# Kernel optimization log

Hardware: AMD Instinct MI355X
Metric: run time of the kernel (lower is better)

Reference implementation:

```python
import jax, jax.numpy as jnp
import numpy as np

N = 100000
IN_PLANES = 64
OUT_PLANES = 64
SHARE = 8
NSAMPLE = 16


def setup_inputs() -> dict:
    key = jax.random.key(0)
    ks = jax.random.split(key, 20)
    f32 = jnp.float32
    s = lambda fan_in: 1.0 / np.sqrt(fan_in)
    inp = {}
    inp['p'] = jax.random.normal(ks[0], (N, 3), f32)
    inp['x'] = jax.random.normal(ks[1], (N, IN_PLANES), f32)
    inp['knn_idx'] = jax.random.randint(ks[2], (N, NSAMPLE), 0, N, jnp.int64)
    # channelMixMLPs01: Linear(3+in, nsample) -> ReLU -> Bilinear(ns, ns, ns)
    inp['W01'] = jax.random.uniform(ks[3], (3 + IN_PLANES, NSAMPLE), f32, -s(3 + IN_PLANES), s(3 + IN_PLANES))
    inp['b01'] = jnp.zeros((NSAMPLE,), f32)
    inp['Wbil'] = jax.random.uniform(ks[4], (NSAMPLE, NSAMPLE, NSAMPLE), f32, -s(NSAMPLE), s(NSAMPLE))
    inp['bbil'] = jnp.zeros((NSAMPLE,), f32)
    # linear_p: Linear(3,3) -> BN(3) -> ReLU -> Linear(3, out)
    inp['Wp1'] = jax.random.uniform(ks[5], (3, 3), f32, -s(3), s(3))
    inp['bp1'] = jnp.zeros((3,), f32)
    inp['bnp_s'] = jnp.ones((3,), f32)   # BN folded (inference): scale = gamma/sqrt(var+eps)
    inp['bnp_b'] = jnp.zeros((3,), f32)  # shift = beta - mean*scale
    inp['Wp2'] = jax.random.uniform(ks[6], (3, OUT_PLANES), f32, -s(3), s(3))
    inp['bp2'] = jnp.zeros((OUT_PLANES,), f32)
    # channelMixMLPs02
    mid = OUT_PLANES
    inp['W2a'] = jax.random.uniform(ks[7], (2 * NSAMPLE, mid), f32, -s(2 * NSAMPLE), s(2 * NSAMPLE))
    inp['bn2a_s'] = jnp.ones((mid,), f32)
    inp['bn2a_b'] = jnp.zeros((mid,), f32)
    inp['W2b'] = jax.random.uniform(ks[8], (mid, mid // SHARE), f32, -s(mid), s(mid))
    inp['bn2b_s'] = jnp.ones((mid // SHARE,), f32)
    inp['bn2b_b'] = jnp.zeros((mid // SHARE,), f32)
    inp['W2c'] = jax.random.uniform(ks[9], (mid // SHARE, OUT_PLANES // SHARE), f32, -s(mid // SHARE), s(mid // SHARE))
    inp['b2c'] = jnp.zeros((OUT_PLANES // SHARE,), f32)
    # channelMixMLPs03: Linear(in, out)
    inp['W3'] = jax.random.uniform(ks[10], (IN_PLANES, OUT_PLANES), f32, -s(IN_PLANES), s(IN_PLANES))
    inp['b3'] = jnp.zeros((OUT_PLANES,), f32)
    return inp


def reference(p, x, knn_idx, W01, b01, Wbil, bbil, Wp1, bp1, bnp_s, bnp_b,
              Wp2, bp2, W2a, bn2a_s, bn2a_b, W2b, bn2b_s, bn2b_b, W2c, b2c,
              W3, b3):
    n, k = knn_idx.shape
    out_planes = W3.shape[1]
    share = SHARE
    # queryandgroup(use_xyz=True): gather neighbors, relative xyz concat features
    p_r = p[knn_idx] - p[:, None, :]                      # [n,k,3]
    x_knn_in = jnp.concatenate([p_r, x[knn_idx]], -1)     # [n,k,3+in]
    xf = x_knn_in.reshape(n * k, -1)
    # channelMixMLPs01: Linear -> ReLU -> Bilinear(e, e)
    e = jax.nn.relu(xf @ W01 + b01)                       # [nk, ns]
    e = jnp.einsum('ni,oij,nj->no', e, Wbil, e) + bbil    # [nk, ns]
    # linear_p on relative coords
    pe = p_r.reshape(-1, 3) @ Wp1 + bp1
    pe = jax.nn.relu(pe * bnp_s + bnp_b)
    pe = pe @ Wp2 + bp2                                   # [nk, out]
    p_embed = pe.reshape(n, k, out_planes)
    # shrink_p: (n k (a b)) -> sum over a -> (nk, b=nsample)
    a = out_planes // k
    shrink = pe.reshape(n * k, a, k).sum(1)               # [nk, ns]
    ef = jnp.concatenate([e, shrink], -1)                 # [nk, 2*ns]
    # channelMixMLPs02
    h = jax.nn.relu((ef @ W2a) * bn2a_s + bn2a_b)
    h = jax.nn.relu((h @ W2b) * bn2b_s + bn2b_b)
    h = h @ W2c + b2c                                     # [nk, out/share]
    w = jax.nn.softmax(h.reshape(n, k, -1), axis=1)       # softmax over neighbors
    # channelMixMLPs03 then gather
    x_v = (x @ W3 + b3)[knn_idx]                          # [n,k,out]
    x_knn = (x_v + p_embed).reshape(n, k, share, out_planes // share)
    x_knn = (x_knn * w[:, :, None, :]).reshape(n, k, out_planes)
    x_out = x_knn.sum(1)                                  # [n,out]
    return (x_out, x_knn, knn_idx, p_r)
```

## Files before the change

kernel.cpp:

```cpp
#include <hip/hip_runtime.h>

#define NPTS 100000
#define NK   1600000

typedef __attribute__((ext_vector_type(8))) short bf16x8;
typedef __attribute__((ext_vector_type(4))) float f32x4;
typedef union { bf16x8 v; unsigned u[4]; } fragu;

#define MFMA(a,b,c) __builtin_amdgcn_mfma_f32_16x16x32_bf16((a),(b),(c),0,0,0)

#define WS_W01  0
#define WS_WBIL 1536
#define WS_W2A  5632
#define WS_W2B  7680
#define WS_WPE  8704

__device__ inline unsigned cvtpk(float lo, float hi) {
  unsigned r;
  asm("v_cvt_pk_bf16_f32 %0, %1, %2" : "=v"(r) : "v"(lo), "v"(hi));
  return r;
}
__device__ inline short bfr(float f) {
  unsigned u = __float_as_uint(f);
  u += 0x7fff + ((u >> 16) & 1);
  return (short)(u >> 16);
}

__global__ __launch_bounds__(256) void k_prep(
    const float* __restrict__ W01, const float* __restrict__ b01,
    const float* __restrict__ Wbil,
    const float* __restrict__ W2a, const float* __restrict__ W2b,
    const float* __restrict__ Wp2, const float* __restrict__ bp2,
    short* __restrict__ ws)
{
  const int t = threadIdx.x;
  for (int i = t; i < 3 * 512; i += 256) {
    int tt = i & 7, l = (i >> 3) & 63, kc = i >> 9;
    int o = l & 15, k = kc * 32 + ((l >> 4) << 3) + tt;
    float v = 0.f;
    if (k < 64) v = W01[(3 + k) * 16 + o];
    else if (k < 67) v = W01[(k - 64) * 16 + o];
    else if (k == 67) v = b01[o];
    ws[WS_W01 + i] = bfr(v);
  }
  for (int i = t; i < 8 * 512; i += 256) {
    int tt = i & 7, l = (i >> 3) & 63, kc = i >> 9;
    int o = l & 15, k = kc * 32 + ((l >> 4) << 3) + tt;
    ws[WS_WBIL + i] = bfr(Wbil[o * 256 + k]);
  }
  for (int i = t; i < 4 * 512; i += 256) {
    int tt = i & 7, l = (i >> 3) & 63, nt = i >> 9;
    int c = nt * 16 + (l & 15), k = ((l >> 4) << 3) + tt;
    ws[WS_W2A + i] = bfr(W2a[k * 64 + c]);
  }
  for (int i = t; i < 2 * 512; i += 256) {
    int tt = i & 7, l = (i >> 3) & 63, kc = i >> 9;
    int m = l & 15, k = kc * 32 + ((l >> 4) << 3) + tt;
    ws[WS_W2B + i] = bfr(m < 8 ? W2b[k * 8 + m] : 0.f);
  }
  for (int i = t; i < 4 * 512; i += 256) {
    int tt = i & 7, l = (i >> 3) & 63, nt = i >> 9;
    int c = nt * 16 + (l & 15), k = ((l >> 4) << 3) + tt;
    float v = 0.f;
    if (k < 3) v = Wp2[k * 64 + c]; else if (k == 3) v = bp2[c];
    ws[WS_WPE + i] = bfr(v);
  }
}

__global__ __launch_bounds__(256) void k_xw3(
    const float* __restrict__ x, const float* __restrict__ W3,
    const float* __restrict__ b3, float* __restrict__ y)
{
  int t = blockIdx.x * 256 + threadIdx.x;
  int i = __builtin_amdgcn_readfirstlane(t >> 6);
  int c = t & 63;
  if (i >= NPTS) return;
  const float* xr = x + i * 64;
  float acc = b3[c];
#pragma unroll
  for (int k = 0; k < 64; ++k)
    acc = fmaf(xr[k], W3[k * 64 + c], acc);
  y[i * 64 + c] = acc;
}

__global__ __launch_bounds__(256, 4) void k_main(
    const float* __restrict__ p, const float* __restrict__ x,
    const int* __restrict__ knn, const short* __restrict__ wsf,
    const float* __restrict__ Wp1, const float* __restrict__ bp1,
    const float* __restrict__ bnp_s, const float* __restrict__ bnp_b,
    const float* __restrict__ bbil,
    const float* __restrict__ bn2a_s, const float* __restrict__ bn2a_b,
    const float* __restrict__ bn2b_s, const float* __restrict__ bn2b_b,
    const float* __restrict__ W2c, const float* __restrict__ b2c,
    const float* __restrict__ Wp2, const float* __restrict__ bp2,
    const float* __restrict__ y,
    float* __restrict__ x_out, float* __restrict__ x_knn)
{
  __shared__ __align__(16) char POOL[40960];

  const int tid  = threadIdx.x;
  const int w    = tid >> 6;
  const int lane = tid & 63;
  const int mloc = lane & 15;
  const int kblk = lane >> 4;
  const int row  = blockIdx.x * 256 + tid;
  const int n    = row >> 4;
  const int j    = row & 15;
  const int idx  = knn[row];

  char* wbase = POOL + w * 10240;
  float* eF  = (float*)wbase;
  short* haS = (short*)wbase;
  float* h2F = (float*)wbase;
  short* efS = (short*)(wbase + 5120);

  const float pr0 = p[idx * 3 + 0] - p[n * 3 + 0];
  const float pr1 = p[idx * 3 + 1] - p[n * 3 + 1];
  const float pr2 = p[idx * 3 + 2] - p[n * 3 + 2];

  float q0, q1, q2;
  {
    float v0 = bp1[0] + pr0 * Wp1[0] + pr1 * Wp1[3] + pr2 * Wp1[6];
    float v1 = bp1[1] + pr0 * Wp1[1] + pr1 * Wp1[4] + pr2 * Wp1[7];
    float v2 = bp1[2] + pr0 * Wp1[2] + pr1 * Wp1[5] + pr2 * Wp1[8];
    q0 = fmaxf(fmaf(v0, bnp_s[0], bnp_b[0]), 0.f);
    q1 = fmaxf(fmaf(v1, bnp_s[1], bnp_b[1]), 0.f);
    q2 = fmaxf(fmaf(v2, bnp_s[2], bnp_b[2]), 0.f);
  }

#define FR(off, idx_) (((const bf16x8*)wsf)[(off) / 8 + (idx_)])

  {
    bf16x8 bw0 = FR(WS_W01, 0 * 64 + lane);
    bf16x8 bw1 = FR(WS_W01, 1 * 64 + lane);
    bf16x8 bw2 = FR(WS_W01, 2 * 64 + lane);
    const float4* x4 = (const float4*)x;
#pragma unroll
    for (int g = 0; g < 4; ++g) {
      const int src = g * 16 + mloc;
      int   ridx = __shfl(idx, src, 64);
      float p0s  = __shfl(pr0, src, 64);
      float p1s  = __shfl(pr1, src, 64);
      float p2s  = __shfl(pr2, src, 64);
      f32x4 acc = {0.f, 0.f, 0.f, 0.f};
      {
        float4 xa = x4[ridx * 16 + kblk * 2];
        float4 xb = x4[ridx * 16 + kblk * 2 + 1];
        fragu A;
        A.u[0] = cvtpk(xa.x, xa.y); A.u[1] = cvtpk(xa.z, xa.w);
        A.u[2] = cvtpk(xb.x, xb.y); A.u[3] = cvtpk(xb.z, xb.w);
        acc = MFMA(A.v, bw0, acc);
      }
      {
        float4 xa = x4[ridx * 16 + 8 + kblk * 2];
        float4 xb = x4[ridx * 16 + 9 + kblk * 2];
        fragu A;
        A.u[0] = cvtpk(xa.x, xa.y); A.u[1] = cvtpk(xa.z, xa.w);
        A.u[2] = cvtpk(xb.x, xb.y); A.u[3] = cvtpk(xb.z, xb.w);
        acc = MFMA(A.v, bw1, acc);
      }
      {
        fragu A;
        A.u[0] = (kblk == 0) ? cvtpk(p0s, p1s) : 0u;
        A.u[1] = (kblk == 0) ? cvtpk(p2s, 1.f) : 0u;
        A.u[2] = 0u; A.u[3] = 0u;
        acc = MFMA(A.v, bw2, acc);
      }
#pragma unroll
      for (int r = 0; r < 4; ++r)
        eF[(g * 16 + kblk * 4 + r) * 20 + mloc] = fmaxf(acc[r], 0.f);
    }
  }

  {
    const float bbo = bbil[mloc];
    const int jh = (kblk & 1), ih = (kblk >> 1);
#pragma unroll 1
    for (int g = 0; g < 4; ++g) {
      const int rl = g * 16 + mloc;
      float er[16];
      *(float4*)&er[0]  = *(const float4*)&eF[rl * 20 + 0];
      *(float4*)&er[4]  = *(const float4*)&eF[rl * 20 + 4];
      *(float4*)&er[8]  = *(const float4*)&eF[rl * 20 + 8];
      *(float4*)&er[12] = *(const float4*)&eF[rl * 20 + 12];
      float ej[8];
#pragma unroll
      for (int t = 0; t < 8; ++t) ej[t] = jh ? er[8 + t] : er[t];
      f32x4 acc = {0.f, 0.f, 0.f, 0.f};
#pragma unroll
      for (int kc = 0; kc < 8; ++kc) {
        bf16x8 wb = FR(WS_WBIL, kc * 64 + lane);
        float ei = ih ? er[kc * 2 + 1] : er[kc * 2];
        fragu A;
        A.u[0] = cvtpk(ei * ej[0], ei * ej[1]);
        A.u[1] = cvtpk(ei * ej[2], ei * ej[3]);
        A.u[2] = cvtpk(ei * ej[4], ei * ej[5]);
        A.u[3] = cvtpk(ei * ej[6], ei * ej[7]);
        acc = MFMA(A.v, wb, acc);
      }
#pragma unroll
      for (int r = 0; r < 4; ++r)
        efS[(g * 16 + kblk * 4 + r) * 40 + mloc] = bfr(acc[r] + bbo);
    }
  }

  {
    bf16x8 wp0 = FR(WS_WPE, 0 * 64 + lane);
    bf16x8 wp1 = FR(WS_WPE, 1 * 64 + lane);
    bf16x8 wp2f = FR(WS_WPE, 2 * 64 + lane);
    bf16x8 wp3 = FR(WS_WPE, 3 * 64 + lane);
#pragma unroll 1
    for (int g = 0; g < 4; ++g) {
      const int src = g * 16 + mloc;
      float q0s = __shfl(q0, src, 64);
      float q1s = __shfl(q1, src, 64);
      float q2s = __shfl(q2, src, 64);
      fragu A;
      A.u[0] = (kblk == 0) ? cvtpk(q0s, q1s) : 0u;
      A.u[1] = (kblk == 0) ? cvtpk(q2s, 1.f) : 0u;
      A.u[2] = 0u; A.u[3] = 0u;
      f32x4 z = {0.f, 0.f, 0.f, 0.f};
      f32x4 s0 = MFMA(A.v, wp0, z);
      f32x4 s1 = MFMA(A.v, wp1, z);
      f32x4 s2 = MFMA(A.v, wp2f, z);
      f32x4 s3 = MFMA(A.v, wp3, z);
#pragma unroll
      for (int r = 0; r < 4; ++r)
        efS[(g * 16 + kblk * 4 + r) * 40 + 16 + mloc] = bfr(s0[r] + s1[r] + s2[r] + s3[r]);
    }
  }

  f32x4 h2acc[4];
#pragma unroll
  for (int g = 0; g < 4; ++g) h2acc[g] = (f32x4){0.f, 0.f, 0.f, 0.f};

#pragma unroll
  for (int half = 0; half < 2; ++half) {
    bf16x8 wa0 = FR(WS_W2A, (half * 2 + 0) * 64 + lane);
    bf16x8 wa1 = FR(WS_W2A, (half * 2 + 1) * 64 + lane);
    float sA = bn2a_s[half * 32 + mloc],      bA = bn2a_b[half * 32 + mloc];
    float sB = bn2a_s[half * 32 + 16 + mloc], bB = bn2a_b[half * 32 + 16 + mloc];
#pragma unroll
    for (int g = 0; g < 4; ++g) {
      const int rl = g * 16 + mloc;
      bf16x8 a = *(const bf16x8*)&efS[rl * 40 + kblk * 8];
      f32x4 z = {0.f, 0.f, 0.f, 0.f};
      f32x4 c0 = MFMA(a, wa0, z);
      f32x4 c1 = MFMA(a, wa1, z);
#pragma unroll
      for (int r = 0; r < 4; ++r) {
        const int rr = g * 16 + kblk * 4 + r;
        haS[rr * 40 + mloc]      = bfr(fmaxf(fmaf(c0[r], sA, bA), 0.f));
        haS[rr * 40 + 16 + mloc] = bfr(fmaxf(fmaf(c1[r], sB, bB), 0.f));
      }
    }
    bf16x8 wbh = FR(WS_W2B, half * 64 + lane);
#pragma unroll
    for (int g = 0; g < 4; ++g) {
      const int rl = g * 16 + mloc;
      bf16x8 a = *(const bf16x8*)&haS[rl * 40 + kblk * 8];
      h2acc[g] = MFMA(a, wbh, h2acc[g]);
    }
  }

  if (mloc < 8) {
    float ss = bn2b_s[mloc], sb = bn2b_b[mloc];
#pragma unroll
    for (int g = 0; g < 4; ++g)
#pragma unroll
      for (int r = 0; r < 4; ++r)
        h2F[(g * 16 + kblk * 4 + r) * 12 + mloc] =
            fmaxf(fmaf(h2acc[g][r], ss, sb), 0.f);
  }

  float h2r[8];
  *(float4*)&h2r[0] = *(const float4*)&h2F[lane * 12 + 0];
  *(float4*)&h2r[4] = *(const float4*)&h2F[lane * 12 + 4];
  float h3[8];
#pragma unroll
  for (int b = 0; b < 8; ++b) h3[b] = b2c[b];
#pragma unroll
  for (int m = 0; m < 8; ++m) {
    float r = h2r[m];
#pragma unroll
    for (int b = 0; b < 8; ++b) h3[b] = fmaf(r, W2c[m * 8 + b], h3[b]);
  }
  float wv[8];
#pragma unroll
  for (int b = 0; b < 8; ++b) {
    float mx = h3[b];
    mx = fmaxf(mx, __shfl_xor(mx, 1, 16));
    mx = fmaxf(mx, __shfl_xor(mx, 2, 16));
    mx = fmaxf(mx, __shfl_xor(mx, 4, 16));
    mx = fmaxf(mx, __shfl_xor(mx, 8, 16));
    float ex = __expf(h3[b] - mx);
    float s = ex;
    s += __shfl_xor(s, 1, 16);
    s += __shfl_xor(s, 2, 16);
    s += __shfl_xor(s, 4, 16);
    s += __shfl_xor(s, 8, 16);
    wv[b] = ex / s;
  }

  const float4* y4 = (const float4*)y;
  float* xkrow = x_knn + (long long)row * 64;
  float xo[4] = {0.f, 0.f, 0.f, 0.f};
#pragma unroll
  for (int h = 0; h < 2; ++h) {
    float4 yv[8];
#pragma unroll
    for (int u = 0; u < 8; ++u) yv[u] = y4[idx * 16 + h * 8 + u];
    f32x4 vout[8];
#pragma unroll
    for (int u = 0; u < 8; ++u) {
      float comp[4] = {yv[u].x, yv[u].y, yv[u].z, yv[u].w};
#pragma unroll
      for (int cc = 0; cc < 4; ++cc) {
        const int c = h * 32 + u * 4 + cc;
        float pe = bp2[c] + q0 * Wp2[c] + q1 * Wp2[64 + c] + q2 * Wp2[128 + c];
        float val = (comp[cc] + pe) * wv[c & 7];
        vout[u][cc] = val;
        float r = val;
        r += __shfl_xor(r, 1, 16);
        r += __shfl_xor(r, 2, 16);
        r += __shfl_xor(r, 4, 16);
        r += __shfl_xor(r, 8, 16);
        if (j == (c & 15)) xo[c >> 4] = r;
      }
    }
#pragma unroll
    for (int u = 0; u < 8; ++u)
      *(f32x4*)(xkrow + h * 32 + u * 4) = vout[u];
  }
#pragma unroll
  for (int g = 0; g < 4; ++g)
    x_out[n * 64 + g * 16 + j] = xo[g];
}

__global__ __launch_bounds__(256) void k_tail(
    const float* __restrict__ p, const int* __restrict__ knn,
    float* __restrict__ knn_f, float* __restrict__ p_r)
{
  int row = blockIdx.x * 256 + threadIdx.x;
  if (row >= NK) return;
  int n = row >> 4;
  int idx = knn[row];
  knn_f[row] = (float)idx;
  p_r[row * 3 + 0] = p[idx * 3 + 0] - p[n * 3 + 0];
  p_r[row * 3 + 1] = p[idx * 3 + 1] - p[n * 3 + 1];
  p_r[row * 3 + 2] = p[idx * 3 + 2] - p[n * 3 + 2];
}

extern "C" void kernel_launch(void* const* d_in, const int* in_sizes, int n_in,
                              void* d_out, int out_size, void* d_ws, size_t ws_size,
                              hipStream_t stream)
{
  const float* p    = (const float*)d_in[0];
  const float* x    = (const float*)d_in[1];
  const int*   knn  = (const int*)d_in[2];
  const float* W01  = (const float*)d_in[3];
  const float* b01  = (const float*)d_in[4];
  const float* Wbil = (const float*)d_in[5];
  const float* bbil = (const float*)d_in[6];
  const float* Wp1  = (const float*)d_in[7];
  const float* bp1  = (const float*)d_in[8];
  const float* bnps = (const float*)d_in[9];
  const float* bnpb = (const float*)d_in[10];
  const float* Wp2  = (const float*)d_in[11];
  const float* bp2  = (const float*)d_in[12];
  const float* W2a  = (const float*)d_in[13];
  const float* s2a  = (const float*)d_in[14];
  const float* b2a  = (const float*)d_in[15];
  const float* W2b  = (const float*)d_in[16];
  const float* s2b  = (const float*)d_in[17];
  const float* b2b  = (const float*)d_in[18];
  const float* W2c  = (const float*)d_in[19];
  const float* b2c  = (const float*)d_in[20];
  const float* W3   = (const float*)d_in[21];
  const float* b3   = (const float*)d_in[22];

  float* outF  = (float*)d_out;
  float* x_out = outF;
  float* x_knn = outF + 6400000;
  float* knn_f = outF + 108800000;
  float* p_r   = outF + 110400000;
  float* y     = knn_f;
  short* wsf   = (short*)d_ws;

  k_prep<<<1, 256, 0, stream>>>(W01, b01, Wbil, W2a, W2b, Wp2, bp2, wsf);
  k_xw3<<<25000, 256, 0, stream>>>(x, W3, b3, y);
  k_main<<<6250, 256, 0, stream>>>(p, x, knn, wsf, Wp1, bp1, bnps, bnpb,
                                   bbil, s2a, b2a, s2b, b2b, W2c, b2c,
                                   Wp2, bp2, y, x_out, x_knn);
  k_tail<<<6250, 256, 0, stream>>>(p, knn, knn_f, p_r);
}
```

Measured before the change: 437.7 us.

## Keep MLP intermediates in registers via transposed MFMA and fuse tail outputs

Swaps the MFMA operand order so each lane owns a row's outputs, then moves intermediates between lanes with shuffles instead of staging them in LDS. The 40 KB shared pool is dropped and the occupancy hint rises from 4 to 5 blocks. When the workspace is large enough, y is kept in the workspace and knn_f/p_r are written from the main kernel, which removes the separate tail launch and its re-gather of p. The cost is many more cross-lane shuffles and extra bf16 rounding of the layer-1 activations.

```diff
diff --git a/kernel.cpp b/kernel.cpp
--- a/kernel.cpp
+++ b/kernel.cpp
@@ -14,6 +14,7 @@
 #define WS_W2A  5632
 #define WS_W2B  7680
 #define WS_WPE  8704
+#define WS_BYTES 21504
 
 __device__ inline unsigned cvtpk(float lo, float hi) {
   unsigned r;
@@ -25,6 +26,8 @@
   u += 0x7fff + ((u >> 16) & 1);
   return (short)(u >> 16);
 }
+__device__ inline float bflo(unsigned u) { return __uint_as_float(u << 16); }
+__device__ inline float bfhi(unsigned u) { return __uint_as_float(u & 0xffff0000u); }
 
 __global__ __launch_bounds__(256) void k_prep(
     const float* __restrict__ W01, const float* __restrict__ b01,
@@ -83,7 +86,7 @@
   y[i * 64 + c] = acc;
 }
 
-__global__ __launch_bounds__(256, 4) void k_main(
+__global__ __launch_bounds__(256, 5) void k_main(
     const float* __restrict__ p, const float* __restrict__ x,
     const int* __restrict__ knn, const short* __restrict__ wsf,
     const float* __restrict__ Wp1, const float* __restrict__ bp1,
@@ -94,12 +97,10 @@
     const float* __restrict__ W2c, const float* __restrict__ b2c,
     const float* __restrict__ Wp2, const float* __restrict__ bp2,
     const float* __restrict__ y,
-    float* __restrict__ x_out, float* __restrict__ x_knn)
+    float* __restrict__ x_out, float* __restrict__ x_knn,
+    float* __restrict__ knn_f, float* __restrict__ p_r)
 {
-  __shared__ __align__(16) char POOL[40960];
-
   const int tid  = threadIdx.x;
-  const int w    = tid >> 6;
   const int lane = tid & 63;
   const int mloc = lane & 15;
   const int kblk = lane >> 4;
@@ -107,12 +108,6 @@
   const int n    = row >> 4;
   const int j    = row & 15;
   const int idx  = knn[row];
-
-  char* wbase = POOL + w * 10240;
-  float* eF  = (float*)wbase;
-  short* haS = (short*)wbase;
-  float* h2F = (float*)wbase;
-  short* efS = (short*)(wbase + 5120);
 
   const float pr0 = p[idx * 3 + 0] - p[n * 3 + 0];
   const float pr1 = p[idx * 3 + 1] - p[n * 3 + 1];
@@ -130,6 +125,7 @@
 
 #define FR(off, idx_) (((const bf16x8*)wsf)[(off) / 8 + (idx_)])
 
+  unsigned epk[4][2];
   {
     bf16x8 bw0 = FR(WS_W01, 0 * 64 + lane);
     bf16x8 bw1 = FR(WS_W01, 1 * 64 + lane);
@@ -146,136 +142,172 @@
       {
         float4 xa = x4[ridx * 16 + kblk * 2];
         float4 xb = x4[ridx * 16 + kblk * 2 + 1];
-        fragu A;
-        A.u[0] = cvtpk(xa.x, xa.y); A.u[1] = cvtpk(xa.z, xa.w);
-        A.u[2] = cvtpk(xb.x, xb.y); A.u[3] = cvtpk(xb.z, xb.w);
-        acc = MFMA(A.v, bw0, acc);
+        fragu B;
+        B.u[0] = cvtpk(xa.x, xa.y); B.u[1] = cvtpk(xa.z, xa.w);
+        B.u[2] = cvtpk(xb.x, xb.y); B.u[3] = cvtpk(xb.z, xb.w);
+        acc = MFMA(bw0, B.v, acc);
       }
       {
         float4 xa = x4[ridx * 16 + 8 + kblk * 2];
         float4 xb = x4[ridx * 16 + 9 + kblk * 2];
-        fragu A;
-        A.u[0] = cvtpk(xa.x, xa.y); A.u[1] = cvtpk(xa.z, xa.w);
-        A.u[2] = cvtpk(xb.x, xb.y); A.u[3] = cvtpk(xb.z, xb.w);
-        acc = MFMA(A.v, bw1, acc);
+        fragu B;
+        B.u[0] = cvtpk(xa.x, xa.y); B.u[1] = cvtpk(xa.z, xa.w);
+        B.u[2] = cvtpk(xb.x, xb.y); B.u[3] = cvtpk(xb.z, xb.w);
+        acc = MFMA(bw1, B.v, acc);
       }
       {
-        fragu A;
-        A.u[0] = (kblk == 0) ? cvtpk(p0s, p1s) : 0u;
-        A.u[1] = (kblk == 0) ? cvtpk(p2s, 1.f) : 0u;
-        A.u[2] = 0u; A.u[3] = 0u;
-        acc = MFMA(A.v, bw2, acc);
-      }
-#pragma unroll
-      for (int r = 0; r < 4; ++r)
-        eF[(g * 16 + kblk * 4 + r) * 20 + mloc] = fmaxf(acc[r], 0.f);
-    }
-  }
-
-  {
-    const float bbo = bbil[mloc];
-    const int jh = (kblk & 1), ih = (kblk >> 1);
-#pragma unroll 1
-    for (int g = 0; g < 4; ++g) {
-      const int rl = g * 16 + mloc;
-      float er[16];
-      *(float4*)&er[0]  = *(const float4*)&eF[rl * 20 + 0];
-      *(float4*)&er[4]  = *(const float4*)&eF[rl * 20 + 4];
-      *(float4*)&er[8]  = *(const float4*)&eF[rl * 20 + 8];
-      *(float4*)&er[12] = *(const float4*)&eF[rl * 20 + 12];
-      float ej[8];
-#pragma unroll
-      for (int t = 0; t < 8; ++t) ej[t] = jh ? er[8 + t] : er[t];
-      f32x4 acc = {0.f, 0.f, 0.f, 0.f};
+        fragu B;
+        B.u[0] = (kblk == 0) ? cvtpk(p0s, p1s) : 0u;
+        B.u[1] = (kblk == 0) ? cvtpk(p2s, 1.f) : 0u;
+        B.u[2] = 0u; B.u[3] = 0u;
+        acc = MFMA(bw2, B.v, acc);
+      }
+      epk[g][0] = cvtpk(fmaxf(acc[0], 0.f), fmaxf(acc[1], 0.f));
+      epk[g][1] = cvtpk(fmaxf(acc[2], 0.f), fmaxf(acc[3], 0.f));
+    }
+  }
+
+  unsigned h2p[4][2];
+#pragma unroll
+  for (int g = 0; g < 4; ++g) {
+    float er[16];
+    {
+      unsigned a0 = __shfl(epk[g][0], mloc, 64);
+      unsigned a1 = __shfl(epk[g][1], mloc, 64);
+      unsigned b0 = __shfl(epk[g][0], mloc + 16, 64);
+      unsigned b1 = __shfl(epk[g][1], mloc + 16, 64);
+      unsigned c0 = __shfl(epk[g][0], mloc + 32, 64);
+      unsigned c1 = __shfl(epk[g][1], mloc + 32, 64);
+      unsigned d0 = __shfl(epk[g][0], mloc + 48, 64);
+      unsigned d1 = __shfl(epk[g][1], mloc + 48, 64);
+      er[0] = bflo(a0);  er[1] = bfhi(a0);  er[2]  = bflo(a1); er[3]  = bfhi(a1);
+      er[4] = bflo(b0);  er[5] = bfhi(b0);  er[6]  = bflo(b1); er[7]  = bfhi(b1);
+      er[8] = bflo(c0);  er[9] = bfhi(c0);  er[10] = bflo(c1); er[11] = bfhi(c1);
+      er[12] = bflo(d0); er[13] = bfhi(d0); er[14] = bflo(d1); er[15] = bfhi(d1);
+    }
+    const int jhsel = kblk & 1, ihsel = kblk >> 1;
+    float ej[8];
+#pragma unroll
+    for (int t = 0; t < 8; ++t) ej[t] = jhsel ? er[8 + t] : er[t];
+    f32x4 acc2;
+    {
+      f32x4 bb = *(const f32x4*)&bbil[kblk * 4];
+      acc2 = bb;
 #pragma unroll
       for (int kc = 0; kc < 8; ++kc) {
         bf16x8 wb = FR(WS_WBIL, kc * 64 + lane);
-        float ei = ih ? er[kc * 2 + 1] : er[kc * 2];
-        fragu A;
-        A.u[0] = cvtpk(ei * ej[0], ei * ej[1]);
-        A.u[1] = cvtpk(ei * ej[2], ei * ej[3]);
-        A.u[2] = cvtpk(ei * ej[4], ei * ej[5]);
-        A.u[3] = cvtpk(ei * ej[6], ei * ej[7]);
-        acc = MFMA(A.v, wb, acc);
-      }
-#pragma unroll
-      for (int r = 0; r < 4; ++r)
-        efS[(g * 16 + kblk * 4 + r) * 40 + mloc] = bfr(acc[r] + bbo);
-    }
-  }
-
-  {
-    bf16x8 wp0 = FR(WS_WPE, 0 * 64 + lane);
-    bf16x8 wp1 = FR(WS_WPE, 1 * 64 + lane);
-    bf16x8 wp2f = FR(WS_WPE, 2 * 64 + lane);
-    bf16x8 wp3 = FR(WS_WPE, 3 * 64 + lane);
-#pragma unroll 1
-    for (int g = 0; g < 4; ++g) {
+        float ei = ihsel ? er[2 * kc + 1] : er[2 * kc];
+        fragu B;
+        B.u[0] = cvtpk(ei * ej[0], ei * ej[1]);
+        B.u[1] = cvtpk(ei * ej[2], ei * ej[3]);
+        B.u[2] = cvtpk(ei * ej[4], ei * ej[5]);
+        B.u[3] = cvtpk(ei * ej[6], ei * ej[7]);
+        acc2 = MFMA(wb, B.v, acc2);
+      }
+    }
+    f32x4 shq;
+    {
       const int src = g * 16 + mloc;
       float q0s = __shfl(q0, src, 64);
       float q1s = __shfl(q1, src, 64);
       float q2s = __shfl(q2, src, 64);
-      fragu A;
-      A.u[0] = (kblk == 0) ? cvtpk(q0s, q1s) : 0u;
-      A.u[1] = (kblk == 0) ? cvtpk(q2s, 1.f) : 0u;
-      A.u[2] = 0u; A.u[3] = 0u;
+      fragu B;
+      B.u[0] = (kblk == 0) ? cvtpk(q0s, q1s) : 0u;
+      B.u[1] = (kblk == 0) ? cvtpk(q2s, 1.f) : 0u;
+      B.u[2] = 0u; B.u[3] = 0u;
       f32x4 z = {0.f, 0.f, 0.f, 0.f};
-      f32x4 s0 = MFMA(A.v, wp0, z);
-      f32x4 s1 = MFMA(A.v, wp1, z);
-      f32x4 s2 = MFMA(A.v, wp2f, z);
-      f32x4 s3 = MFMA(A.v, wp3, z);
-#pragma unroll
-      for (int r = 0; r < 4; ++r)
-        efS[(g * 16 + kblk * 4 + r) * 40 + 16 + mloc] = bfr(s0[r] + s1[r] + s2[r] + s3[r]);
-    }
-  }
-
-  f32x4 h2acc[4];
-#pragma unroll
-  for (int g = 0; g < 4; ++g) h2acc[g] = (f32x4){0.f, 0.f, 0.f, 0.f};
-
-#pragma unroll
-  for (int half = 0; half < 2; ++half) {
-    bf16x8 wa0 = FR(WS_W2A, (half * 2 + 0) * 64 + lane);
-    bf16x8 wa1 = FR(WS_W2A, (half * 2 + 1) * 64 + lane);
-    float sA = bn2a_s[half * 32 + mloc],      bA = bn2a_b[half * 32 + mloc];
-    float sB = bn2a_s[half * 32 + 16 + mloc], bB = bn2a_b[half * 32 + 16 + mloc];
-#pragma unroll
-    for (int g = 0; g < 4; ++g) {
-      const int rl = g * 16 + mloc;
-      bf16x8 a = *(const bf16x8*)&efS[rl * 40 + kblk * 8];
+      f32x4 s0 = MFMA(FR(WS_WPE, 0 * 64 + lane), B.v, z);
+      f32x4 s1 = MFMA(FR(WS_WPE, 1 * 64 + lane), B.v, z);
+      f32x4 s2 = MFMA(FR(WS_WPE, 2 * 64 + lane), B.v, z);
+      f32x4 s3 = MFMA(FR(WS_WPE, 3 * 64 + lane), B.v, z);
+#pragma unroll
+      for (int r = 0; r < 4; ++r) shq[r] = s0[r] + s1[r] + s2[r] + s3[r];
+    }
+    unsigned pe2_0 = cvtpk(acc2[0], acc2[1]);
+    unsigned pe2_1 = cvtpk(acc2[2], acc2[3]);
+    unsigned psh_0 = cvtpk(shq[0], shq[1]);
+    unsigned psh_1 = cvtpk(shq[2], shq[3]);
+    fragu Bef;
+    {
+      const int s1l = mloc + 32 * (kblk & 1);
+      const int s2l = s1l + 16;
+      unsigned a0 = __shfl(pe2_0, s1l, 64);
+      unsigned a1 = __shfl(pe2_1, s1l, 64);
+      unsigned a2 = __shfl(pe2_0, s2l, 64);
+      unsigned a3 = __shfl(pe2_1, s2l, 64);
+      unsigned b0 = __shfl(psh_0, s1l, 64);
+      unsigned b1 = __shfl(psh_1, s1l, 64);
+      unsigned b2 = __shfl(psh_0, s2l, 64);
+      unsigned b3 = __shfl(psh_1, s2l, 64);
+      const bool lo2 = (kblk < 2);
+      Bef.u[0] = lo2 ? a0 : b0; Bef.u[1] = lo2 ? a1 : b1;
+      Bef.u[2] = lo2 ? a2 : b2; Bef.u[3] = lo2 ? a3 : b3;
+    }
+    unsigned pha[8];
+#pragma unroll
+    for (int nt = 0; nt < 4; ++nt) {
+      bf16x8 wa = FR(WS_W2A, nt * 64 + lane);
       f32x4 z = {0.f, 0.f, 0.f, 0.f};
-      f32x4 c0 = MFMA(a, wa0, z);
-      f32x4 c1 = MFMA(a, wa1, z);
-#pragma unroll
-      for (int r = 0; r < 4; ++r) {
-        const int rr = g * 16 + kblk * 4 + r;
-        haS[rr * 40 + mloc]      = bfr(fmaxf(fmaf(c0[r], sA, bA), 0.f));
-        haS[rr * 40 + 16 + mloc] = bfr(fmaxf(fmaf(c1[r], sB, bB), 0.f));
-      }
-    }
-    bf16x8 wbh = FR(WS_W2B, half * 64 + lane);
-#pragma unroll
-    for (int g = 0; g < 4; ++g) {
-      const int rl = g * 16 + mloc;
-      bf16x8 a = *(const bf16x8*)&haS[rl * 40 + kblk * 8];
-      h2acc[g] = MFMA(a, wbh, h2acc[g]);
-    }
-  }
-
-  if (mloc < 8) {
-    float ss = bn2b_s[mloc], sb = bn2b_b[mloc];
-#pragma unroll
-    for (int g = 0; g < 4; ++g)
-#pragma unroll
-      for (int r = 0; r < 4; ++r)
-        h2F[(g * 16 + kblk * 4 + r) * 12 + mloc] =
-            fmaxf(fmaf(h2acc[g][r], ss, sb), 0.f);
-  }
-
+      f32x4 c = MFMA(wa, Bef.v, z);
+      f32x4 sA = *(const f32x4*)&bn2a_s[nt * 16 + kblk * 4];
+      f32x4 bA = *(const f32x4*)&bn2a_b[nt * 16 + kblk * 4];
+      float h0 = fmaxf(fmaf(c[0], sA[0], bA[0]), 0.f);
+      float h1 = fmaxf(fmaf(c[1], sA[1], bA[1]), 0.f);
+      float h2 = fmaxf(fmaf(c[2], sA[2], bA[2]), 0.f);
+      float h3 = fmaxf(fmaf(c[3], sA[3], bA[3]), 0.f);
+      pha[nt * 2 + 0] = cvtpk(h0, h1);
+      pha[nt * 2 + 1] = cvtpk(h2, h3);
+    }
+    {
+      const int sAl = mloc + 32 * (kblk & 1);
+      const int sBl = sAl + 16;
+      const bool lo2 = (kblk < 2);
+      fragu B0, B1;
+      {
+        unsigned a0 = __shfl(pha[0], sAl, 64), a1 = __shfl(pha[1], sAl, 64);
+        unsigned a2 = __shfl(pha[0], sBl, 64), a3 = __shfl(pha[1], sBl, 64);
+        unsigned b0 = __shfl(pha[2], sAl, 64), b1 = __shfl(pha[3], sAl, 64);
+        unsigned b2 = __shfl(pha[2], sBl, 64), b3 = __shfl(pha[3], sBl, 64);
+        B0.u[0] = lo2 ? a0 : b0; B0.u[1] = lo2 ? a1 : b1;
+        B0.u[2] = lo2 ? a2 : b2; B0.u[3] = lo2 ? a3 : b3;
+      }
+      {
+        unsigned a0 = __shfl(pha[4], sAl, 64), a1 = __shfl(pha[5], sAl, 64);
+        unsigned a2 = __shfl(pha[4], sBl, 64), a3 = __shfl(pha[5], sBl, 64);
+        unsigned b0 = __shfl(pha[6], sAl, 64), b1 = __shfl(pha[7], sAl, 64);
+        unsigned b2 = __shfl(pha[6], sBl, 64), b3 = __shfl(pha[7], sBl, 64);
+        B1.u[0] = lo2 ? a0 : b0; B1.u[1] = lo2 ? a1 : b1;
+        B1.u[2] = lo2 ? a2 : b2; B1.u[3] = lo2 ? a3 : b3;
+      }
+      f32x4 acc3 = {0.f, 0.f, 0.f, 0.f};
+      acc3 = MFMA(FR(WS_W2B, 0 * 64 + lane), B0.v, acc3);
+      acc3 = MFMA(FR(WS_W2B, 1 * 64 + lane), B1.v, acc3);
+      f32x4 s = *(const f32x4*)&bn2b_s[(kblk & 1) * 4];
+      f32x4 b = *(const f32x4*)&bn2b_b[(kblk & 1) * 4];
+      float v0 = fmaxf(fmaf(acc3[0], s[0], b[0]), 0.f);
+      float v1 = fmaxf(fmaf(acc3[1], s[1], b[1]), 0.f);
+      float v2 = fmaxf(fmaf(acc3[2], s[2], b[2]), 0.f);
+      float v3 = fmaxf(fmaf(acc3[3], s[3], b[3]), 0.f);
+      h2p[g][0] = cvtpk(v0, v1);
+      h2p[g][1] = cvtpk(v2, v3);
+    }
+  }
+
+  unsigned hp0 = 0, hp1 = 0, hp2 = 0, hp3 = 0;
+#pragma unroll
+  for (int g = 0; g < 4; ++g) {
+    unsigned t0 = __shfl(h2p[g][0], mloc, 64);
+    unsigned t1 = __shfl(h2p[g][1], mloc, 64);
+    unsigned t2 = __shfl(h2p[g][0], mloc + 16, 64);
+    unsigned t3 = __shfl(h2p[g][1], mloc + 16, 64);
+    const bool mine = (kblk == g);
+    hp0 = mine ? t0 : hp0; hp1 = mine ? t1 : hp1;
+    hp2 = mine ? t2 : hp2; hp3 = mine ? t3 : hp3;
+  }
   float h2r[8];
-  *(float4*)&h2r[0] = *(const float4*)&h2F[lane * 12 + 0];
-  *(float4*)&h2r[4] = *(const float4*)&h2F[lane * 12 + 4];
+  h2r[0] = bflo(hp0); h2r[1] = bfhi(hp0); h2r[2] = bflo(hp1); h2r[3] = bfhi(hp1);
+  h2r[4] = bflo(hp2); h2r[5] = bfhi(hp2); h2r[6] = bflo(hp3); h2r[7] = bfhi(hp3);
+
   float h3[8];
 #pragma unroll
   for (int b = 0; b < 8; ++b) h3[b] = b2c[b];
@@ -335,6 +367,13 @@
 #pragma unroll
   for (int g = 0; g < 4; ++g)
     x_out[n * 64 + g * 16 + j] = xo[g];
+
+  if (knn_f) {
+    knn_f[row] = (float)idx;
+    p_r[row * 3 + 0] = pr0;
+    p_r[row * 3 + 1] = pr1;
+    p_r[row * 3 + 2] = pr2;
+  }
 }
 
 __global__ __launch_bounds__(256) void k_tail(
@@ -384,13 +423,19 @@
   float* x_knn = outF + 6400000;
   float* knn_f = outF + 108800000;
   float* p_r   = outF + 110400000;
-  float* y     = knn_f;
   short* wsf   = (short*)d_ws;
+
+  const size_t yBytes = (size_t)NPTS * 64 * sizeof(float);
+  const bool bigWs = ws_size >= (size_t)WS_BYTES + yBytes;
+  float* y = bigWs ? (float*)((char*)d_ws + WS_BYTES) : knn_f;
 
   k_prep<<<1, 256, 0, stream>>>(W01, b01, Wbil, W2a, W2b, Wp2, bp2, wsf);
   k_xw3<<<25000, 256, 0, stream>>>(x, W3, b3, y);
   k_main<<<6250, 256, 0, stream>>>(p, x, knn, wsf, Wp1, bp1, bnps, bnpb,
                                    bbil, s2a, b2a, s2b, b2b, W2c, b2c,
-                                   Wp2, bp2, y, x_out, x_knn);
-  k_tail<<<6250, 256, 0, stream>>>(p, knn, knn_f, p_r);
-}
+                                   Wp2, bp2, y, x_out, x_knn,
+                                   bigWs ? knn_f : (float*)nullptr,
+                                   bigWs ? p_r : (float*)nullptr);
+  if (!bigWs)
+    k_tail<<<6250, 256, 0, stream>>>(p, knn, knn_f, p_r);
+}
```

New measurement: 417.2 us. -4.7%, faster.
